# Kernel tuning notes

Measured on AMD Instinct MI355X. Metric: run time of the kernel, lower is better.

Reference implementation:

```python
import jax, jax.numpy as jnp
import numpy as np
jax.config.update("jax_enable_x64", True)

B, M, L, K = 64, 64, 64, 10


def _diag_sums_upper(A, m):
    # u[b,k] = sum_i A[b, i, i+k]  (sum of k-th upper diagonal), k = 0..m-1
    i = jnp.arange(m)
    k = jnp.arange(m)
    cols = i[None, :] + k[:, None]          # (k, i)
    mask = cols < m
    vals = A[:, i[None, :], jnp.where(mask, cols, 0)]  # (B, m, m)
    return jnp.sum(vals * mask, axis=-1)


def _toeplitz(u):
    # Hermitian-Toeplitz from generator u (B, m): T[i,j] = u[j-i] for j>=i, conj(u[i-j]) for j<i
    m = u.shape[-1]
    left = u[:, 1:][:, ::-1]                                  # u_{m-1}..u_1
    right = jnp.concatenate([u[:, :1], jnp.conj(u[:, 1:])], axis=1)
    full = jnp.concatenate([left, right], axis=1)             # (B, 2m-1)
    idx = (m - 1) + (jnp.arange(m)[:, None] - jnp.arange(m)[None, :])
    return full[:, idx]


def _psd_step(rho, T, X, W, Lamda, key):
    # NO_layer: stack -> random Hermitian perturbation in detached eigenbasis -> PSD projection
    Xh = jnp.conj(jnp.swapaxes(X, 1, 2))
    StackM = jnp.concatenate([
        jnp.concatenate([T, X], axis=2),
        jnp.concatenate([Xh, W], axis=2)], axis=1)
    Theta = -Lamda / rho + StackM
    _, V = jnp.linalg.eigh(jax.lax.stop_gradient(Theta))
    minv = jax.random.normal(key, Theta.shape[:2]).astype(Theta.dtype)
    Theta = Theta + jnp.einsum('bij,bj,bkj->bik', V, minv, jnp.conj(V))
    w, V2 = jnp.linalg.eigh(Theta)
    wpos = jnp.where(w > 0, w, 0.0).astype(Theta.dtype)   # keep strictly positive eigvals only
    Sita = jnp.einsum('bij,bj,bkj->bik', V2, wpos, jnp.conj(V2))
    Sita = (Sita + jnp.conj(jnp.swapaxes(Sita, 1, 2))) * 0.5
    return Sita, StackM


def _forward(Y, rho, tau, eta):
    b, m, l = Y.shape
    n = m + l
    cd = jnp.complex128
    Theta = jnp.zeros((b, n, n), cd)
    Lamda = jnp.zeros((b, n, n), cd)
    IL = jnp.eye(l, dtype=cd)
    norm = (1.0 / jnp.arange(m, 0, -1)).astype(jnp.float64)   # 1/(m-k)
    key = jax.random.key(42)
    T = None
    for it in range(K):
        r = rho[it].astype(jnp.float64)
        t = tau[it].astype(jnp.float64)
        e = eta[it].astype(jnp.float64)
        # RC_layer
        X = (Y + 2.0 * Lamda[:, :m, m:] + 2.0 * r * Theta[:, :m, m:]) / (1.0 + 2.0 * r)
        # AU_layer
        W = Lamda[:, m:, m:] / r + Theta[:, m:, m:] - (t / (2.0 * r)) * IL
        # TO_layer: u = (1/r)*normalizer*(toepadj(Lamda)+r*toepadj(Theta) - (t/2)*m*e1)
        adj = _diag_sums_upper(Lamda[:, :m, :m], m) + r * _diag_sums_upper(Theta[:, :m, :m], m)
        adj = adj.at[:, 0].add(-(t / 2.0) * m)
        u = (norm / r) * adj
        T = _toeplitz(u)
        # NO_layer
        Theta, StackM = _psd_step(r, T, X, W, Lamda, jax.random.fold_in(key, it))
        # MU_layer
        Lamda = Lamda + e * (Theta - StackM)
    # final uvec: means of lower diagonals of T_new: uvec[k] = sum_{j>=k} T[j, j-k] / (m-k)
    i = jnp.arange(m)
    k = jnp.arange(m)
    cols = i[None, :] - k[:, None]
    mask = cols >= 0
    vals = T[:, i[None, :], jnp.where(mask, cols, 0)]
    uvec = jnp.sum(vals * mask, axis=-1) * norm
    return T, uvec


def setup_inputs() -> dict:
    key = jax.random.key(0)
    k1, k2 = jax.random.split(key)
    Y_real = jax.random.normal(k1, (B, M, L), dtype=jnp.float32)
    Y_imag = jax.random.normal(k2, (B, M, L), dtype=jnp.float32)
    rho = jnp.full((K,), 0.5, dtype=jnp.float32)
    tau = jnp.full((K,), 0.5, dtype=jnp.float32)
    eta = jnp.full((K,), 0.1, dtype=jnp.float32)
    return {"Y_real": Y_real, "Y_imag": Y_imag, "rho": rho, "tau": tau, "eta": eta}


def reference(Y_real, Y_imag, rho, tau, eta):
    Y = (Y_real.astype(jnp.float64) + 1j * Y_imag.astype(jnp.float64)).astype(jnp.complex128)
    return _forward(Y, rho, tau, eta)
```

## Files before the change

### kernel.cpp

```cpp
#include <hip/hip_runtime.h>
#include <stdint.h>


#define BATCH 64
#define MDIM 64
#define LDIM 64
#define NDIM 128
#define NSQ (NDIM * NDIM)
#define KITER 10
#define SWEEPS 7
#define RSA 129
#define JAC_LDS_BYTES (NDIM * RSA * (int)sizeof(float2))
#define RCH 12
#define OUT_ELEMS 266240

__device__ __forceinline__ void tf_block(unsigned k0, unsigned k1,
                                         unsigned& x0, unsigned& x1) {
  unsigned k2 = k0 ^ k1 ^ 0x1BD11BDAu;
  x0 += k0; x1 += k1;
#define TF_R(r) { x0 += x1; x1 = (x1 << (r)) | (x1 >> (32 - (r))); x1 ^= x0; }
  TF_R(13) TF_R(15) TF_R(26) TF_R(6)
  x0 += k1; x1 += k2 + 1u;
  TF_R(17) TF_R(29) TF_R(16) TF_R(24)
  x0 += k2; x1 += k0 + 2u;
  TF_R(13) TF_R(15) TF_R(26) TF_R(6)
  x0 += k0; x1 += k1 + 3u;
  TF_R(17) TF_R(29) TF_R(16) TF_R(24)
  x0 += k1; x1 += k2 + 4u;
  TF_R(13) TF_R(15) TF_R(26) TF_R(6)
  x0 += k2; x1 += k0 + 5u;
#undef TF_R
}

__device__ double erfinv_d(double x) {
  double w = -log1p(-x * x);
  double p;
  if (w < 6.25) {
    w -= 3.125;
    const double c[23] = {
      -3.6444120640178196996e-21, -1.685059138182016589e-19,
      1.2858480715256400167e-18,  1.115787767802518096e-17,
      -1.333171662854620906e-16,  2.0972767875968561637e-17,
      6.6376381343583238325e-15,  -4.0545662729752068639e-14,
      -8.1519341976054721522e-14, 2.6335093153082322977e-12,
      -1.2975133253453532498e-11, -5.4154120542946279317e-11,
      1.051212273321532285e-09,   -4.1126339803469836976e-09,
      -2.9070369957882005086e-08, 4.2347877827932403518e-07,
      -1.3654692000834678645e-06, -1.3882523362786468719e-05,
      1.8673420803405714802e-04,  -7.4070253416626697512e-04,
      -6.0336708714301490533e-03, 2.4015818242558961693e-01,
      1.6536545626831027356e+00};
    p = c[0];
#pragma unroll
    for (int i = 1; i < 23; ++i) p = p * w + c[i];
  } else if (w < 16.0) {
    double s = sqrt(w) - 3.25;
    const double c[19] = {
      2.2137376921775787049e-09,  9.0756561938885390979e-08,
      -2.7517406297064545428e-07, 1.8239629214389227755e-08,
      1.5027403968909827627e-06,  -4.013867526981545969e-06,
      2.9234449089955446044e-06,  1.2475304481671778723e-05,
      -4.7318229009055733981e-05, 6.8284851459573175448e-05,
      2.4031110387097893999e-05,  -3.5503752036284748449e-04,
      9.5328937973738049703e-04,  -1.6882755560235047313e-03,
      2.4914420961078508066e-03,  -3.7512085075692412107e-03,
      5.3709145535900636051e-03,  1.0052589676941592334e+00,
      3.0838856104922207635e+00};
    p = c[0];
#pragma unroll
    for (int i = 1; i < 19; ++i) p = p * s + c[i];
  } else {
    double s = sqrt(w) - 5.0;
    const double c[17] = {
      -2.7109920616438573243e-11, -2.5556418169965252055e-10,
      1.5076572693500548083e-09,  -3.7894654401267369937e-09,
      7.6157012080783393804e-09,  -1.4960026627149240478e-08,
      2.9147953450901080826e-08,  -6.7711997758452339498e-08,
      2.2900482228026654717e-07,  -9.9298272942317002539e-07,
      4.5260625972231537039e-06,  -1.9681778105531670567e-05,
      7.5995277030017761139e-05,  -2.1503011930044477347e-04,
      -1.3871931833623122026e-04, 1.0103004648645343977e+00,
      4.8499064014085844221e+00};
    p = c[0];
#pragma unroll
    for (int i = 1; i < 17; ++i) p = p * s + c[i];
  }
  double z = p * x;
  const double spi2 = 0.8862269254527580;
  double ax = fabs(x);
#pragma unroll
  for (int nr = 0; nr < 2; ++nr) {
    if (ax > 0.9375) {
      double az = fabs(z);
      double corr = (erfc(az) - (1.0 - ax)) * spi2 * exp(az * az);
      az += corr;
      z = copysign(az, x);
    } else {
      z -= (erf(z) - x) * spi2 * exp(z * z);
    }
  }
  return z;
}

__global__ void zero_kernel(double* p, size_t n) {
  size_t i = (size_t)blockIdx.x * blockDim.x + threadIdx.x;
  size_t stride = (size_t)gridDim.x * blockDim.x;
  for (; i < n; i += stride) p[i] = 0.0;
}

__global__ void flags_zero_kernel(unsigned* flags) {
  int tid = threadIdx.x;
  if (tid < BATCH * SWEEPS) flags[tid] = 0u;
}

__global__ void prng_kernel(double* minv) {
  int tid = blockIdx.x * blockDim.x + threadIdx.x;
  if (tid >= KITER * BATCH * NDIM) return;
  int it = tid / (BATCH * NDIM);
  int i = tid % (BATCH * NDIM);
  unsigned nk0 = 0u, nk1 = (unsigned)it;
  tf_block(0u, 42u, nk0, nk1);
  unsigned c0 = 0u, c1 = (unsigned)i;
  tf_block(nk0, nk1, c0, c1);
  unsigned long long bits = ((unsigned long long)c0 << 32) | (unsigned long long)c1;
  unsigned long long fb = (bits >> 12) | 0x3FF0000000000000ull;
  double f = __builtin_bit_cast(double, fb) - 1.0;
  const double lo = __builtin_bit_cast(double, 0xBFEFFFFFFFFFFFFFull);
  double uu = f * 2.0 + lo;
  if (uu < lo) uu = lo;
  minv[tid] = 1.4142135623730951 * erfinv_d(uu);
}

__global__ void compute_u_kernel(const double2* Theta, const double2* Lamda,
                                 const float* rho, const float* tau, int it,
                                 double2* u) {
  int tid = blockIdx.x * blockDim.x + threadIdx.x;
  if (tid >= BATCH * MDIM) return;
  int b = tid / MDIM, kk = tid % MDIM;
  double r = (double)rho[it], t = (double)tau[it];
  const double2* Lb = Lamda + (size_t)b * NSQ;
  const double2* Tb = Theta + (size_t)b * NSQ;
  double ar = 0.0, ai = 0.0;
  for (int i = 0; i + kk < MDIM; ++i) {
    double2 L = Lb[i * NDIM + i + kk];
    double2 Th = Tb[i * NDIM + i + kk];
    ar += L.x + r * Th.x;
    ai += L.y + r * Th.y;
  }
  if (kk == 0) ar += -(t * 0.5) * (double)MDIM;
  double s = 1.0 / ((double)(MDIM - kk) * r);
  u[b * MDIM + kk] = make_double2(ar * s, ai * s);
}

__global__ void assemble_kernel(const double2* Theta, const double2* Lamda,
                                const double2* u, const float* Yre, const float* Yim,
                                const float* rho, const float* tau, int it,
                                float2* A32) {
  int tid = blockIdx.x * 256 + threadIdx.x;
  if (tid >= BATCH * NSQ) return;
  int b = tid / NSQ, rem = tid % NSQ, i = rem / NDIM, j = rem % NDIM;
  double r = (double)rho[it], t = (double)tau[it];
  size_t idx = (size_t)b * NSQ + rem;
  double2 L = Lamda[idx], Th = Theta[idx];
  double axr, axi;
  if (i < MDIM && j < MDIM) {
    int d = j - i;
    double2 uv = u[b * MDIM + (d >= 0 ? d : -d)];
    double uy = (d >= 0) ? uv.y : -uv.y;
    axr = uv.x - L.x / r;
    axi = uy - L.y / r;
  } else if (i < MDIM) {
    double yr = (double)Yre[(b * MDIM + i) * LDIM + (j - MDIM)];
    double yi = (double)Yim[(b * MDIM + i) * LDIM + (j - MDIM)];
    double inv = 1.0 / (1.0 + 2.0 * r);
    axr = (yr + 2.0 * L.x + 2.0 * r * Th.x) * inv - L.x / r;
    axi = (yi + 2.0 * L.y + 2.0 * r * Th.y) * inv - L.y / r;
  } else if (j < MDIM) {
    double yr = (double)Yre[(b * MDIM + j) * LDIM + (i - MDIM)];
    double yi = -(double)Yim[(b * MDIM + j) * LDIM + (i - MDIM)];
    double inv = 1.0 / (1.0 + 2.0 * r);
    axr = (yr + 2.0 * L.x + 2.0 * r * Th.x) * inv - L.x / r;
    axi = (yi + 2.0 * L.y + 2.0 * r * Th.y) * inv - L.y / r;
  } else {
    axr = Th.x - ((i == j) ? t / (2.0 * r) : 0.0);
    axi = Th.y;
  }
  A32[idx] = make_float2((float)axr, (float)axi);
}

__device__ __forceinline__ int pair_p(int j, int r) {
  return (j == 0) ? 0 : 1 + (j - 1 + r) % 127;
}
__device__ __forceinline__ int pair_q(int j, int r) {
  return 1 + (126 - j + r) % 127;
}

__device__ __forceinline__ float2 ldc2(const float2* sA, int r, int c) {
  int rr = r <= c ? r : c, cc = r <= c ? c : r;
  float2 v = sA[rr * RSA + cc];
  if (r > c) v.y = -v.y;
  return v;
}
__device__ __forceinline__ void stc2(float2* sA, int r, int c, float zr, float zi) {
  int rr = r <= c ? r : c, cc = r <= c ? c : r;
  sA[rr * RSA + cc] = make_float2(zr, (r <= c) ? zi : -zi);
}

__device__ __forceinline__ void bar_lgkm() {
  asm volatile("s_waitcnt lgkmcnt(0)" ::: "memory");
  __builtin_amdgcn_s_barrier();
}

__global__ __launch_bounds__(1024) void combined_all_kernel(
    const float2* __restrict__ A, float2* __restrict__ U,
    float2* __restrict__ prm,
    unsigned* __restrict__ flags,
    const double* __restrict__ minv, int it,
    double* __restrict__ d1, double* __restrict__ d2) {
  extern __shared__ float smem[];
  int tid = threadIdx.x;

  if (blockIdx.x >= BATCH) {
    if (tid >= 512) return;
    int rb = blockIdx.x - BATCH;
    int wv = tid >> 6, ln = tid & 63;
    int b = rb >> 1, half = rb & 1;
    int col0 = (half * 8 + wv) * 8;
    float* cre = smem + wv * (2 * NDIM * RCH);
    float* cim = cre + NDIM * RCH;
    for (int e = ln; e < NDIM * 8; e += 64) {
      int row = e >> 3, c = e & 7;
      cre[row * RCH + c] = (row == col0 + c) ? 1.0f : 0.0f;
      cim[row * RCH + c] = 0.0f;
    }
    for (int s = 0; s < SWEEPS; ++s) {
      const float2* Pg = prm + ((size_t)s * BATCH + b) * (127 * 64);
      if (ln == 0) {
        while (__hip_atomic_load(&flags[b * SWEEPS + s], __ATOMIC_ACQUIRE,
                                 __HIP_MEMORY_SCOPE_AGENT) != (unsigned)(it + 1)) {
          __builtin_amdgcn_s_sleep(8);
        }
      }
      float2 prmv = Pg[ln];
      for (int r0 = 0; r0 < 127; ++r0) {
        int r = (s & 1) ? (126 - r0) : r0;
        int p = pair_p(ln, r), q = pair_q(ln, r);
        float2 nxt = prmv;
        if (r0 < 126) nxt = Pg[(r0 + 1) * 64 + ln];
        float br = prmv.x, bi = prmv.y;
        float cc = sqrtf(fmaxf(0.0f, 1.0f - br * br - bi * bi));
        float4* Rp = (float4*)(cre + p * RCH);
        float4* Rq = (float4*)(cre + q * RCH);
        float4* Ip = (float4*)(cim + p * RCH);
        float4* Iq = (float4*)(cim + q * RCH);
        float4 pr0 = Rp[0], pr1 = Rp[1], pim0 = Ip[0], pim1 = Ip[1];
        float4 qr0 = Rq[0], qr1 = Rq[1], qim0 = Iq[0], qim1 = Iq[1];
#define ROTC(UPX, UPY, UQX, UQY) { float upx = UPX, upy = UPY, uqx = UQX, uqy = UQY; \
    UPX = cc * upx + (br * uqx + bi * uqy);         \
    UPY = cc * upy + (br * uqy - bi * uqx);                                          \
    UQX = cc * uqx - (br * upx - bi * upy);               \
    UQY = cc * uqy - (br * upy + bi * upx); }
        ROTC(pr0.x, pim0.x, qr0.x, qim0.x)
        ROTC(pr0.y, pim0.y, qr0.y, qim0.y)
        ROTC(pr0.z, pim0.z, qr0.z, qim0.z)
        ROTC(pr0.w, pim0.w, qr0.w, qim0.w)
        ROTC(pr1.x, pim1.x, qr1.x, qim1.x)
        ROTC(pr1.y, pim1.y, qr1.y, qim1.y)
        ROTC(pr1.z, pim1.z, qr1.z, qim1.z)
        ROTC(pr1.w, pim1.w, qr1.w, qim1.w)
#undef ROTC
        Rp[0] = pr0; Rp[1] = pr1; Ip[0] = pim0; Ip[1] = pim1;
        Rq[0] = qr0; Rq[1] = qr1; Iq[0] = qim0; Iq[1] = qim1;
        prmv = nxt;
        __builtin_amdgcn_wave_barrier();
      }
    }
    float2* Ug = U + (size_t)b * NSQ;
    for (int e = ln; e < NDIM * 8; e += 64) {
      int row = e >> 3, c = e & 7;
      Ug[row * NDIM + col0 + c] = make_float2(cre[row * RCH + c], cim[row * RCH + c]);
    }
    return;
  }

  float2* sA2 = (float2*)smem;
  __shared__ float4 sprm2[2][64];
  int b = blockIdx.x;
  const float2* Ag = A + (size_t)b * NSQ;
  for (int i = tid; i < NSQ; i += 1024) {
    sA2[(i >> 7) * RSA + (i & 127)] = Ag[i];
  }
  bool hasband = (tid >= 64 && tid < 64 + 189);
  int bb_i = 0, bb_j = 0;
  if (hasband) {
    int e = tid - 64;
    if (e < 64)       { bb_i = e;      bb_j = e; }
    else if (e < 127) { bb_i = e - 64; bb_j = bb_i + 1; }
    else              { bb_i = e - 127; bb_j = bb_i + 2; }
  }
  int nrest = 0;
  int rb_i[2], rb_j[2];
  rb_i[0] = rb_i[1] = 0; rb_j[0] = rb_j[1] = 0;
  if (tid >= 64) {
#pragma unroll
    for (int m = 0; m < 2; ++m) {
      int e = (tid - 64) + 960 * m;
      if (e < 1891) {
        int i = 0;
        while (i < 60 && (61 * (i + 1) - ((i + 1) * i) / 2) <= e) ++i;
        rb_i[nrest] = i;
        rb_j[nrest] = i + 3 + (e - (61 * i - (i * (i - 1)) / 2));
        ++nrest;
      }
    }
  }
  __syncthreads();

  for (int s = 0; s < SWEEPS; ++s) {
    float2* Pg = prm + ((size_t)s * BATCH + b) * (127 * 64);
    const bool fwd = !(s & 1);
    const int r_init = fwd ? 0 : 126;
    auto stepP = [&](int x) {
      return fwd ? ((x == 0) ? 0 : ((x == 127) ? 1 : x + 1))
                 : ((x == 0) ? 0 : ((x == 1) ? 127 : x - 1));
    };
    auto stepQ = [&](int x) {
      return fwd ? ((x == 127) ? 1 : x + 1)
                 : ((x == 1) ? 127 : x - 1);
    };
    int bpi = pair_p(bb_i, r_init), bqi = pair_q(bb_i, r_init);
    int bpj = pair_p(bb_j, r_init), bqj = pair_q(bb_j, r_init);
    int rpi[2], rqi[2], rpj[2], rqj[2];
#pragma unroll
    for (int m = 0; m < 2; ++m) {
      rpi[m] = pair_p(rb_i[m], r_init); rqi[m] = pair_q(rb_i[m], r_init);
      rpj[m] = pair_p(rb_j[m], r_init); rqj[m] = pair_q(rb_j[m], r_init);
    }
    auto pcalc = [&](int pp, int qq, int buf, int pos) {
      float app = sA2[pp * RSA + pp].x, aqq = sA2[qq * RSA + qq].x;
      float2 g = ldc2(sA2, pp, qq);
      float ag2 = g.x * g.x + g.y * g.y;
      float cc = 1.0f, br = 0.0f, bi = 0.0f;
      if (ag2 > 1e-24f) {
        float ag = sqrtf(ag2);
        float ta = (aqq - app) / (2.0f * ag);
        float tt = -copysignf(1.0f, ta) / (fabsf(ta) + sqrtf(1.0f + ta * ta));
        cc = 1.0f / sqrtf(1.0f + tt * tt);
        float tcag = tt * cc / ag;
        br = g.x * tcag; bi = g.y * tcag;
      }
      sprm2[buf][tid] = make_float4(cc, br, bi, 0.0f);
      Pg[pos * 64 + tid] = make_float2(br, bi);
    };
    auto rot = [&](int bi_s, int bj_s, int pi_, int qi_, int pj_, int qj_, int buf) {
      float2 B00 = ldc2(sA2, pi_, pj_);
      float2 B01 = ldc2(sA2, pi_, qj_);
      float2 B10 = ldc2(sA2, qi_, pj_);
      float2 B11 = ldc2(sA2, qi_, qj_);
      float4 Pi = sprm2[buf][bi_s], Pj = sprm2[buf][bj_s];
      float ci = Pi.x, bri = Pi.y, bii = Pi.z;
      float cj = Pj.x, brj = Pj.y, bij = Pj.z;
      float t00r = ci * B00.x + (bri * B10.x - bii * B10.y);
      float t00i = ci * B00.y + (bri * B10.y + bii * B10.x);
      float t01r = ci * B01.x + (bri * B11.x - bii * B11.y);
      float t01i = ci * B01.y + (bri * B11.y + bii * B11.x);
      float t10r = ci * B10.x - (bri * B00.x + bii * B00.y);
      float t10i = ci * B10.y - (bri * B00.y - bii * B00.x);
      float t11r = ci * B11.x - (bri * B01.x + bii * B01.y);
      float t11i = ci * B11.y - (bri * B01.y - bii * B01.x);
      stc2(sA2, pi_, pj_,
           cj * t00r + (brj * t01r + bij * t01i),
           cj * t00i + (brj * t01i - bij * t01r));
      stc2(sA2, pi_, qj_,
           cj * t01r - (brj * t00r - bij * t00i),
           cj * t01i - (brj * t00i + bij * t00r));
      stc2(sA2, qi_, pj_,
           cj * t10r + (brj * t11r + bij * t11i),
           cj * t10i + (brj * t11i - bij * t11r));
      stc2(sA2, qi_, qj_,
           cj * t11r - (brj * t10r - bij * t10i),
           cj * t11i - (brj * t10i + bij * t10r));
    };
    int ppn = 0, qqn = 0;
    if (tid < 64) {
      int pp0 = pair_p(tid, r_init), qq0 = pair_q(tid, r_init);
      pcalc(pp0, qq0, 0, 0);
      ppn = stepP(pp0); qqn = stepQ(qq0);
    }
    bar_lgkm();
    int cur = 0;
    for (int r0 = 0; r0 < 127; ++r0) {
      if (hasband) rot(bb_i, bb_j, bpi, bqi, bpj, bqj, cur);
      bar_lgkm();
      if (tid < 64) {
        if (r0 < 126) {
          pcalc(ppn, qqn, cur ^ 1, r0 + 1);
          ppn = stepP(ppn); qqn = stepQ(qqn);
        }
      } else {
        if (nrest > 0) rot(rb_i[0], rb_j[0], rpi[0], rqi[0], rpj[0], rqj[0], cur);
        if (nrest > 1) rot(rb_i[1], rb_j[1], rpi[1], rqi[1], rpj[1], rqj[1], cur);
      }
      bar_lgkm();
      cur ^= 1;
      bpi = stepP(bpi); bqi = stepQ(bqi); bpj = stepP(bpj); bqj = stepQ(bqj);
#pragma unroll
      for (int m = 0; m < 2; ++m) {
        rpi[m] = stepP(rpi[m]); rqi[m] = stepQ(rqi[m]);
        rpj[m] = stepP(rpj[m]); rqj[m] = stepQ(rqj[m]);
      }
    }
    if (tid == 0) {
      __hip_atomic_store(&flags[b * SWEEPS + s], (unsigned)(it + 1),
                         __ATOMIC_RELEASE, __HIP_MEMORY_SCOPE_AGENT);
    }
  }

  if (tid < NDIM) {
    float wj = sA2[tid * RSA + tid].x;
    int rank = 0;
    for (int k2 = 0; k2 < NDIM; ++k2) {
      float wk = sA2[k2 * RSA + k2].x;
      rank += (wk < wj) || (wk == wj && k2 < tid);
    }
    double mv = minv[(it * BATCH + b) * NDIM + rank];
    double v = (double)wj + mv;
    if (v < 0.0) v = 0.0;
    d1[b * NDIM + tid] = v;
    d2[b * NDIM + tid] = v - (double)wj;
  }
}

__global__ __launch_bounds__(256) void update_kernel(
    const float2* U, const double* d1, const double* d2,
    const float* rho, const float* eta, int it,
    double2* Theta, double2* Lamda) {
  __shared__ float ViRe[32][33], ViIm[32][33];
  __shared__ float VkRe[32][33], VkIm[32][33];
  __shared__ double s1[32], s2[32];
  int blk = blockIdx.x;
  int b = blk >> 4, tile = blk & 15, ti = tile >> 2, tk = tile & 3;
  int tid = threadIdx.x;
  int lk = tid & 31, lig = tid >> 5;
  double r = (double)rho[it], e = (double)eta[it];
  double a1x[4] = {0, 0, 0, 0}, a1y[4] = {0, 0, 0, 0};
  double a2x[4] = {0, 0, 0, 0}, a2y[4] = {0, 0, 0, 0};
  const float2* Ub = U + (size_t)b * NSQ;
  for (int jc = 0; jc < 4; ++jc) {
    for (int e2 = tid; e2 < 1024; e2 += 256) {
      int rr = e2 & 31, cc2 = e2 >> 5;
      float2 v1 = Ub[(jc * 32 + cc2) * NDIM + ti * 32 + rr];
      ViRe[rr][cc2] = v1.x; ViIm[rr][cc2] = v1.y;
      float2 v2 = Ub[(jc * 32 + cc2) * NDIM + tk * 32 + rr];
      VkRe[rr][cc2] = v2.x; VkIm[rr][cc2] = v2.y;
    }
    if (tid < 32) {
      s1[tid] = d1[b * NDIM + jc * 32 + tid];
      s2[tid] = d2[b * NDIM + jc * 32 + tid];
    }
    __syncthreads();
#pragma unroll
    for (int uo = 0; uo < 4; ++uo) {
      int li = lig + uo * 8;
      double ax = a1x[uo], ay = a1y[uo], bx = a2x[uo], by = a2y[uo];
      for (int jj = 0; jj < 32; ++jj) {
        float var = ViRe[li][jj], vai = ViIm[li][jj];
        float vbr = VkRe[lk][jj], vbi = VkIm[lk][jj];
        double pr = (double)(var * vbr + vai * vbi);
        double pi = (double)(vai * vbr - var * vbi);
        ax += s1[jj] * pr; ay += s1[jj] * pi;
        bx += s2[jj] * pr; by += s2[jj] * pi;
      }
      a1x[uo] = ax; a1y[uo] = ay; a2x[uo] = bx; a2y[uo] = by;
    }
    __syncthreads();
  }
  double lf = 1.0 - e / r;
#pragma unroll
  for (int uo = 0; uo < 4; ++uo) {
    int gi = ti * 32 + lig + uo * 8, gk = tk * 32 + lk;
    size_t idx = (size_t)b * NSQ + gi * NDIM + gk;
    Theta[idx] = make_double2(a1x[uo], a1y[uo]);
    double2 Lold = Lamda[idx];
    Lamda[idx] = make_double2(lf * Lold.x + e * a2x[uo], lf * Lold.y + e * a2y[uo]);
  }
}

__global__ void writeout_kernel(const double2* u, float* out) {
  int tid = blockIdx.x * 256 + threadIdx.x;
  if (tid >= OUT_ELEMS) return;
  double re;
  if (tid < BATCH * MDIM * MDIM) {
    int b = tid >> 12, rem = tid & 4095, i = rem >> 6, j = rem & 63;
    int d = j - i;
    re = u[b * MDIM + (d >= 0 ? d : -d)].x;
  } else {
    int k2 = tid - BATCH * MDIM * MDIM;
    int b = k2 >> 6, kk = k2 & 63;
    re = u[b * MDIM + kk].x;
  }
  out[tid] = (float)re;
}

extern "C" void kernel_launch(void* const* d_in, const int* in_sizes, int n_in,
                              void* d_out, int out_size, void* d_ws, size_t ws_size,
                              hipStream_t stream) {
  const float* Yre = (const float*)d_in[0];
  const float* Yim = (const float*)d_in[1];
  const float* rho = (const float*)d_in[2];
  const float* tau = (const float*)d_in[3];
  const float* eta = (const float*)d_in[4];
  float* out = (float*)d_out;

  char* ws = (char*)d_ws;
  size_t off = 0;
  auto take = [&](size_t bytes) -> char* {
    char* p = ws + off;
    off += (bytes + 255) & ~(size_t)255;
    return p;
  };
  double2* u     = (double2*)take((size_t)BATCH * MDIM * sizeof(double2));
  double*  minv  = (double*)take((size_t)KITER * BATCH * NDIM * sizeof(double));
  double*  d1    = (double*)take((size_t)BATCH * NDIM * sizeof(double));
  double*  d2    = (double*)take((size_t)BATCH * NDIM * sizeof(double));
  double2* Lamda = (double2*)take((size_t)BATCH * NSQ * sizeof(double2));
  double2* Theta = (double2*)take((size_t)BATCH * NSQ * sizeof(double2));
  float2*  A32   = (float2*)take((size_t)BATCH * NSQ * sizeof(float2));
  float2*  U32   = (float2*)take((size_t)BATCH * NSQ * sizeof(float2));
  float2*  prm   = (float2*)take((size_t)SWEEPS * BATCH * 127 * 64 * sizeof(float2));
  unsigned* flags = (unsigned*)take((size_t)BATCH * SWEEPS * sizeof(unsigned));
  (void)in_sizes; (void)n_in; (void)ws_size; (void)out_size;

  hipFuncSetAttribute((const void*)combined_all_kernel,
                      hipFuncAttributeMaxDynamicSharedMemorySize, JAC_LDS_BYTES);

  zero_kernel<<<2048, 256, 0, stream>>>((double*)Theta, (size_t)BATCH * NSQ * 2);
  zero_kernel<<<2048, 256, 0, stream>>>((double*)Lamda, (size_t)BATCH * NSQ * 2);
  flags_zero_kernel<<<1, 512, 0, stream>>>(flags);
  prng_kernel<<<(KITER * BATCH * NDIM + 255) / 256, 256, 0, stream>>>(minv);

  for (int it = 0; it < KITER - 1; ++it) {
    compute_u_kernel<<<16, 256, 0, stream>>>(Theta, Lamda, rho, tau, it, u);
    assemble_kernel<<<BATCH * NSQ / 256, 256, 0, stream>>>(Theta, Lamda, u, Yre, Yim,
                                                           rho, tau, it, A32);
    combined_all_kernel<<<BATCH + 2 * BATCH, 1024, JAC_LDS_BYTES, stream>>>(
        A32, U32, prm, flags, minv, it, d1, d2);
    update_kernel<<<BATCH * 16, 256, 0, stream>>>(U32, d1, d2, rho, eta, it, Theta, Lamda);
  }
  compute_u_kernel<<<16, 256, 0, stream>>>(Theta, Lamda, rho, tau, KITER - 1, u);
  writeout_kernel<<<(OUT_ELEMS + 255) / 256, 256, 0, stream>>>(u, out);
}
```

Baseline: 15.90 ms.

## Move band rotations to wave 0 and drop a barrier per Jacobi round

Wave 0 now applies the three diagonal-band block rotations itself, then computes the next round's rotation parameters, with only a wave barrier in between. This removes one block-wide barrier from each of the 127 rounds per sweep. The other waves load all four matrix entries for both of their off-band rotations before doing the arithmetic, so more LDS reads are in flight at once. The LDS row stride changes from 129 to 130 to alter bank mapping. In exchange, wave 0 carries more serial work each round and may become the critical path.

```diff
diff --git a/kernel.cpp b/kernel.cpp
--- a/kernel.cpp
+++ b/kernel.cpp
@@ -9,7 +9,7 @@
 #define NSQ (NDIM * NDIM)
 #define KITER 10
 #define SWEEPS 7
-#define RSA 129
+#define RSA 130
 #define JAC_LDS_BYTES (NDIM * RSA * (int)sizeof(float2))
 #define RCH 12
 #define OUT_ELEMS 266240
@@ -290,14 +290,6 @@
   for (int i = tid; i < NSQ; i += 1024) {
     sA2[(i >> 7) * RSA + (i & 127)] = Ag[i];
   }
-  bool hasband = (tid >= 64 && tid < 64 + 189);
-  int bb_i = 0, bb_j = 0;
-  if (hasband) {
-    int e = tid - 64;
-    if (e < 64)       { bb_i = e;      bb_j = e; }
-    else if (e < 127) { bb_i = e - 64; bb_j = bb_i + 1; }
-    else              { bb_i = e - 127; bb_j = bb_i + 2; }
-  }
   int nrest = 0;
   int rb_i[2], rb_j[2];
   rb_i[0] = rb_i[1] = 0; rb_j[0] = rb_j[1] = 0;
@@ -314,6 +306,7 @@
       }
     }
   }
+  int ln = tid;
   __syncthreads();
 
   for (int s = 0; s < SWEEPS; ++s) {
@@ -328,8 +321,9 @@
       return fwd ? ((x == 127) ? 1 : x + 1)
                  : ((x == 1) ? 127 : x - 1);
     };
-    int bpi = pair_p(bb_i, r_init), bqi = pair_q(bb_i, r_init);
-    int bpj = pair_p(bb_j, r_init), bqj = pair_q(bb_j, r_init);
+    int bp0 = pair_p(ln, r_init), bq0 = pair_q(ln, r_init);
+    int bp1 = pair_p(ln + 1, r_init), bq1 = pair_q(ln + 1, r_init);
+    int bp2 = pair_p(ln + 2, r_init), bq2 = pair_q(ln + 2, r_init);
     int rpi[2], rqi[2], rpj[2], rqj[2];
 #pragma unroll
     for (int m = 0; m < 2; ++m) {
@@ -381,6 +375,32 @@
            cj * t11r - (brj * t10r - bij * t10i),
            cj * t11i - (brj * t10i + bij * t10r));
     };
+    auto rotc = [&](int bi_s, int bj_s, int pi_, int qi_, int pj_, int qj_, int buf,
+                    float2 B00, float2 B01, float2 B10, float2 B11) {
+      float4 Pi = sprm2[buf][bi_s], Pj = sprm2[buf][bj_s];
+      float ci = Pi.x, bri = Pi.y, bii = Pi.z;
+      float cj = Pj.x, brj = Pj.y, bij = Pj.z;
+      float t00r = ci * B00.x + (bri * B10.x - bii * B10.y);
+      float t00i = ci * B00.y + (bri * B10.y + bii * B10.x);
+      float t01r = ci * B01.x + (bri * B11.x - bii * B11.y);
+      float t01i = ci * B01.y + (bri * B11.y + bii * B11.x);
+      float t10r = ci * B10.x - (bri * B00.x + bii * B00.y);
+      float t10i = ci * B10.y - (bri * B00.y - bii * B00.x);
+      float t11r = ci * B11.x - (bri * B01.x + bii * B01.y);
+      float t11i = ci * B11.y - (bri * B01.y - bii * B01.x);
+      stc2(sA2, pi_, pj_,
+           cj * t00r + (brj * t01r + bij * t01i),
+           cj * t00i + (brj * t01i - bij * t01r));
+      stc2(sA2, pi_, qj_,
+           cj * t01r - (brj * t00r - bij * t00i),
+           cj * t01i - (brj * t00i + bij * t00r));
+      stc2(sA2, qi_, pj_,
+           cj * t10r + (brj * t11r + bij * t11i),
+           cj * t10i + (brj * t11i - bij * t11r));
+      stc2(sA2, qi_, qj_,
+           cj * t11r - (brj * t10r - bij * t10i),
+           cj * t11i - (brj * t10i + bij * t10r));
+    };
     int ppn = 0, qqn = 0;
     if (tid < 64) {
       int pp0 = pair_p(tid, r_init), qq0 = pair_q(tid, r_init);
@@ -390,20 +410,41 @@
     bar_lgkm();
     int cur = 0;
     for (int r0 = 0; r0 < 127; ++r0) {
-      if (hasband) rot(bb_i, bb_j, bpi, bqi, bpj, bqj, cur);
-      bar_lgkm();
       if (tid < 64) {
+        rot(ln, ln, bp0, bq0, bp0, bq0, cur);
+        if (ln <= 62) rot(ln, ln + 1, bp0, bq0, bp1, bq1, cur);
+        if (ln <= 61) rot(ln, ln + 2, bp0, bq0, bp2, bq2, cur);
+        __builtin_amdgcn_wave_barrier();
         if (r0 < 126) {
           pcalc(ppn, qqn, cur ^ 1, r0 + 1);
           ppn = stepP(ppn); qqn = stepQ(qqn);
         }
       } else {
-        if (nrest > 0) rot(rb_i[0], rb_j[0], rpi[0], rqi[0], rpj[0], rqj[0], cur);
-        if (nrest > 1) rot(rb_i[1], rb_j[1], rpi[1], rqi[1], rpj[1], rqj[1], cur);
+        float2 B00a, B01a, B10a, B11a, B00b, B01b, B10b, B11b;
+        if (nrest > 0) {
+          B00a = ldc2(sA2, rpi[0], rpj[0]);
+          B01a = ldc2(sA2, rpi[0], rqj[0]);
+          B10a = ldc2(sA2, rqi[0], rpj[0]);
+          B11a = ldc2(sA2, rqi[0], rqj[0]);
+        }
+        if (nrest > 1) {
+          B00b = ldc2(sA2, rpi[1], rpj[1]);
+          B01b = ldc2(sA2, rpi[1], rqj[1]);
+          B10b = ldc2(sA2, rqi[1], rpj[1]);
+          B11b = ldc2(sA2, rqi[1], rqj[1]);
+        }
+        if (nrest > 0)
+          rotc(rb_i[0], rb_j[0], rpi[0], rqi[0], rpj[0], rqj[0], cur,
+               B00a, B01a, B10a, B11a);
+        if (nrest > 1)
+          rotc(rb_i[1], rb_j[1], rpi[1], rqi[1], rpj[1], rqj[1], cur,
+               B00b, B01b, B10b, B11b);
       }
       bar_lgkm();
       cur ^= 1;
-      bpi = stepP(bpi); bqi = stepQ(bqi); bpj = stepP(bpj); bqj = stepQ(bqj);
+      bp0 = stepP(bp0); bq0 = stepQ(bq0);
+      bp1 = stepP(bp1); bq1 = stepQ(bq1);
+      bp2 = stepP(bp2); bq2 = stepQ(bq2);
 #pragma unroll
       for (int m = 0; m < 2; ++m) {
         rpi[m] = stepP(rpi[m]); rqi[m] = stepQ(rqi[m]);
```

Result: faster. 14.63 ms, median of 2 (-7.9%).
